# Optimization experiments

Measured on AMD Instinct MI355X. Metric: run time of the kernel, lower is better.

Reference implementation:

```python
import jax, jax.numpy as jnp
import numpy as np

# Key insight: 'take the first candidate in descending-score order that is not yet
# used' is exactly 'argmax of the score over unused items'. Since vocab == 25 and
# every index has a char, the Python fallback branch is unreachable for
# seq_len <= vocab. So the whole greedy dedup collapses to a masked-argmax scan
# over positions, vectorized across the batch.

def setup_inputs() -> dict:
    key = jax.random.key(0)
    B, S, V = 65536, 25, 25
    matrix = jax.random.normal(key, (B, S, V), dtype=jnp.float32)
    return {"matrix": matrix}


def reference(matrix):
    B, S, V = matrix.shape
    neg = jnp.finfo(matrix.dtype).min

    def step(used, scores):  # used: [B,V] bool, scores: [B,V]
        masked = jnp.where(used, neg, scores)
        sel = jnp.argmax(masked, axis=-1)                       # [B] greedy pick
        val = jnp.take_along_axis(scores, sel[:, None], axis=-1)[:, 0]
        used = used | jax.nn.one_hot(sel, V, dtype=bool)        # mark as used
        return used, (sel, val)

    used0 = jnp.zeros((B, V), dtype=bool)
    _, (sels, vals) = jax.lax.scan(step, used0, jnp.swapaxes(matrix, 0, 1))
    # actions: [B,S] int32 item ids (== char index, char = chr(id + ord('A')))
    actions = jnp.swapaxes(sels, 0, 1).astype(jnp.int32)
    sel_scores = jnp.swapaxes(vals, 0, 1)                        # [B,S] float
    return actions, sel_scores
```

## Files before the change

kernel.cpp:

```cpp
#include <hip/hip_runtime.h>
#include <stdint.h>


#define S_LEN 25
#define VOCAB 25
#define ROWS_PER_BLOCK 256
#define THREADS 256
#define WAVES 4
#define DW_PER_STEP (ROWS_PER_BLOCK * VOCAB)
#define DW_PER_WAVE (DW_PER_STEP / WAVES)
#define J_ITERS (DW_PER_WAVE / 64)

__device__ __forceinline__ void gld_dword(const float* g, float* l) {
  __builtin_amdgcn_global_load_lds(
      (const __attribute__((address_space(1))) void*)g,
      (__attribute__((address_space(3))) void*)l, 4, 0, 0);
}

__global__ __launch_bounds__(THREADS) void greedy_dedup_kernel(
    const float* __restrict__ m, float* __restrict__ out, int B) {
  __shared__ float buf[2][DW_PER_STEP];
  __shared__ float actbuf[DW_PER_STEP];
  __shared__ float valbuf[DW_PER_STEP];

  const int t = threadIdx.x;
  const int lane = t & 63;
  const int wv = t >> 6;
  const long long blk0 = (long long)blockIdx.x * ROWS_PER_BLOCK;
  const float* bb = m + blk0 * (S_LEN * VOCAB);

  const float* ga[J_ITERS];
#pragma unroll
  for (int j = 0; j < J_ITERS; ++j) {
    int linear = wv * DW_PER_WAVE + j * 64 + lane;
    int row = linear / VOCAB;
    int v = linear - row * VOCAB;
    ga[j] = bb + row * (S_LEN * VOCAB) + v;
  }

#pragma unroll
  for (int j = 0; j < J_ITERS; ++j) {
    gld_dword(ga[j], &buf[0][wv * DW_PER_WAVE + j * 64]);
    ga[j] += VOCAB;
  }
  __syncthreads();

  unsigned used = 0u;
  for (int s = 0; s < S_LEN; ++s) {
    if (s + 1 < S_LEN) {
      float* dst = buf[(s + 1) & 1];
#pragma unroll
      for (int j = 0; j < J_ITERS; ++j) {
        gld_dword(ga[j], &dst[wv * DW_PER_WAVE + j * 64]);
        ga[j] += VOCAB;
      }
    }

    const float* src = buf[s & 1] + t * VOCAB;
    float best = -3.402823466e38f;
    int bi = 0;
#pragma unroll
    for (int v = 0; v < VOCAB; ++v) {
      float x = src[v];
      bool free_v = ((used >> v) & 1u) == 0u;
      if (free_v && x > best) { best = x; bi = v; }
    }
    used |= (1u << bi);
    actbuf[t * VOCAB + s] = (float)bi;
    valbuf[t * VOCAB + s] = best;
    __syncthreads();
  }

  float* gact = out + blk0 * S_LEN;
  float* gval = out + (long long)B * S_LEN + blk0 * S_LEN;
#pragma unroll
  for (int k = 0; k < S_LEN; ++k) {
    int idx = t + k * THREADS;
    gact[idx] = actbuf[idx];
    gval[idx] = valbuf[idx];
  }
}

extern "C" void kernel_launch(void* const* d_in, const int* in_sizes, int n_in,
                              void* d_out, int out_size, void* d_ws, size_t ws_size,
                              hipStream_t stream) {
  const float* m = (const float*)d_in[0];
  float* out = (float*)d_out;
  int B = in_sizes[0] / (S_LEN * VOCAB);
  int grid = B / ROWS_PER_BLOCK;
  greedy_dedup_kernel<<<grid, THREADS, 0, stream>>>(m, out, B);
}
```

Measured before the change: 244.5 us.

## Use single-wave blocks with register-staged prefetch instead of direct-to-LDS loads

Shrinks each block to one 64-thread wave handling 64 rows, and replaces the global_load_lds direct-to-shared loads with ordinary global loads into registers. Those registers are written into the other LDS buffer after the per-row argmax work. The smaller block makes the per-step barrier cheaper and gives four times as many blocks to spread across CUs. In exchange it uses 25 registers for the prefetch, adds a VGPR-to-LDS store pass each step, and issues extra load instructions.

```diff
diff --git a/kernel.cpp b/kernel.cpp
--- a/kernel.cpp
+++ b/kernel.cpp
@@ -4,56 +4,43 @@
 
 #define S_LEN 25
 #define VOCAB 25
-#define ROWS_PER_BLOCK 256
-#define THREADS 256
-#define WAVES 4
-#define DW_PER_STEP (ROWS_PER_BLOCK * VOCAB)
-#define DW_PER_WAVE (DW_PER_STEP / WAVES)
-#define J_ITERS (DW_PER_WAVE / 64)
+#define ROWS 64
+#define SLICE (ROWS * VOCAB)
+#define J_ITERS (SLICE / 64)
 
-__device__ __forceinline__ void gld_dword(const float* g, float* l) {
-  __builtin_amdgcn_global_load_lds(
-      (const __attribute__((address_space(1))) void*)g,
-      (__attribute__((address_space(3))) void*)l, 4, 0, 0);
-}
-
-__global__ __launch_bounds__(THREADS) void greedy_dedup_kernel(
+__global__ __launch_bounds__(64) void greedy_dedup_kernel(
     const float* __restrict__ m, float* __restrict__ out, int B) {
-  __shared__ float buf[2][DW_PER_STEP];
-  __shared__ float actbuf[DW_PER_STEP];
-  __shared__ float valbuf[DW_PER_STEP];
+  __shared__ float buf[2][SLICE];
+  __shared__ float abuf[SLICE];
+  __shared__ float vbuf[SLICE];
 
   const int t = threadIdx.x;
-  const int lane = t & 63;
-  const int wv = t >> 6;
-  const long long blk0 = (long long)blockIdx.x * ROWS_PER_BLOCK;
-  const float* bb = m + blk0 * (S_LEN * VOCAB);
+  const long long blk0 = (long long)blockIdx.x * ROWS;
+  const float* base = m + blk0 * (S_LEN * VOCAB);
 
-  const float* ga[J_ITERS];
+  int off0[J_ITERS];
 #pragma unroll
   for (int j = 0; j < J_ITERS; ++j) {
-    int linear = wv * DW_PER_WAVE + j * 64 + lane;
-    int row = linear / VOCAB;
-    int v = linear - row * VOCAB;
-    ga[j] = bb + row * (S_LEN * VOCAB) + v;
+    int q = j * 64 + t;
+    int row = q / VOCAB;
+    int v = q - row * VOCAB;
+    off0[j] = row * (S_LEN * VOCAB) + v;
   }
 
+  float pf[J_ITERS];
+
 #pragma unroll
-  for (int j = 0; j < J_ITERS; ++j) {
-    gld_dword(ga[j], &buf[0][wv * DW_PER_WAVE + j * 64]);
-    ga[j] += VOCAB;
-  }
+  for (int j = 0; j < J_ITERS; ++j) pf[j] = base[off0[j]];
+#pragma unroll
+  for (int j = 0; j < J_ITERS; ++j) buf[0][j * 64 + t] = pf[j];
   __syncthreads();
 
   unsigned used = 0u;
   for (int s = 0; s < S_LEN; ++s) {
     if (s + 1 < S_LEN) {
-      float* dst = buf[(s + 1) & 1];
+      const int soff = (s + 1) * VOCAB;
 #pragma unroll
-      for (int j = 0; j < J_ITERS; ++j) {
-        gld_dword(ga[j], &dst[wv * DW_PER_WAVE + j * 64]);
-        ga[j] += VOCAB;
-      }
+      for (int j = 0; j < J_ITERS; ++j) pf[j] = base[off0[j] + soff];
     }
 
     const float* src = buf[s & 1] + t * VOCAB;
@@ -66,18 +53,24 @@
       if (free_v && x > best) { best = x; bi = v; }
     }
     used |= (1u << bi);
-    actbuf[t * VOCAB + s] = (float)bi;
-    valbuf[t * VOCAB + s] = best;
+    abuf[t * VOCAB + s] = (float)bi;
+    vbuf[t * VOCAB + s] = best;
+
+    if (s + 1 < S_LEN) {
+      float* dst = buf[(s + 1) & 1];
+#pragma unroll
+      for (int j = 0; j < J_ITERS; ++j) dst[j * 64 + t] = pf[j];
+    }
     __syncthreads();
   }
 
   float* gact = out + blk0 * S_LEN;
   float* gval = out + (long long)B * S_LEN + blk0 * S_LEN;
 #pragma unroll
-  for (int k = 0; k < S_LEN; ++k) {
-    int idx = t + k * THREADS;
-    gact[idx] = actbuf[idx];
-    gval[idx] = valbuf[idx];
+  for (int k = 0; k < J_ITERS; ++k) {
+    int idx = k * 64 + t;
+    gact[idx] = abuf[idx];
+    gval[idx] = vbuf[idx];
   }
 }
 
@@ -87,6 +80,6 @@
   const float* m = (const float*)d_in[0];
   float* out = (float*)d_out;
   int B = in_sizes[0] / (S_LEN * VOCAB);
-  int grid = B / ROWS_PER_BLOCK;
-  greedy_dedup_kernel<<<grid, THREADS, 0, stream>>>(m, out, B);
+  int grid = B / ROWS;
+  greedy_dedup_kernel<<<grid, ROWS, 0, stream>>>(m, out, B);
 }
```

New measurement: 232.6 us. -4.8%, faster.
